# Optimization experiments

Measured on AMD Instinct MI355X. Metric: run time of the kernel, lower is better.

Reference implementation:

```python
import jax, jax.numpy as jnp
import numpy as np

B, M, N, C = 1, 128, 256, 256
MID, OUT_C = 32, 128
LN_EPS = 1e-5
NORM_EPS = 1e-3


def setup_inputs() -> dict:
    key = jax.random.key(0)
    ks = jax.random.split(key, 9)
    act = jax.random.normal(ks[0], (B, M, N, C), dtype=jnp.float32)
    mask = (jax.random.uniform(ks[1], (B, M, N)) < 0.9).astype(jnp.float32)
    s_in = 1.0 / np.sqrt(C)
    s_mid = 1.0 / np.sqrt(MID * MID)
    return {
        "act": act,
        "mask": mask,
        "ln_g": jnp.ones((C,), jnp.float32),
        "ln_b": jnp.zeros((C,), jnp.float32),
        "lw": jax.random.normal(ks[2], (MID, C), jnp.float32) * s_in,
        "lb": jnp.zeros((MID,), jnp.float32),
        "rw": jax.random.normal(ks[3], (MID, C), jnp.float32) * s_in,
        "rb": jnp.zeros((MID,), jnp.float32),
        "ow": jax.random.normal(ks[4], (OUT_C, MID * MID), jnp.float32) * s_mid,
        "ob": jnp.zeros((OUT_C,), jnp.float32),
    }


def reference(act, mask, ln_g, ln_b, lw, lb, rw, rb, ow, ob):
    # LayerNorm over channel dim
    mu = jnp.mean(act, axis=-1, keepdims=True)
    var = jnp.mean(jnp.square(act - mu), axis=-1, keepdims=True)
    x = (act - mu) * jax.lax.rsqrt(var + LN_EPS) * ln_g + ln_b  # [b,m,i,c]

    m = mask[..., None]  # [b,m,i,1]
    left = m * (jnp.einsum('bmic,xc->bmix', x, lw) + lb)   # [b,m,i,mid]
    right = m * (jnp.einsum('bmic,yc->bmiy', x, rw) + rb)  # [b,m,i,mid]

    # outer product mean over MSA dim m -> [b,i,j,x,y]
    x2d = jnp.einsum('bmix,bmjy->bijxy', left, right)
    x2d = x2d.reshape(x2d.shape[:3] + (MID * MID,))
    out = jnp.einsum('bijk,ok->bijo', x2d, ow) + ob  # [b,i,j,out_c]

    norm = jnp.einsum('bmi,bmj->bij', mask, mask)[..., None]
    return out / (norm + NORM_EPS)
```

## Files before the change

kernel.cpp:

```cpp
#include <hip/hip_runtime.h>
#include <hip/hip_bf16.h>

typedef __bf16 bf16x8 __attribute__((ext_vector_type(8)));
typedef __bf16 bf16x4 __attribute__((ext_vector_type(4)));
typedef float  f32x4  __attribute__((ext_vector_type(4)));

#define MDIM 128
#define NDIM 256
#define CDIM 256
#define MIDC 32
#define OUTC 128

#define LSX_RS 1156
#define LSX_YS 36
#define LSX_BYTES (64 * LSX_RS * 2)

__global__ __launch_bounds__(256) void prep_kernel(
    const float* __restrict__ mask,
    const float* __restrict__ lw, const float* __restrict__ lb,
    const float* __restrict__ rw, const float* __restrict__ rb,
    const float* __restrict__ ow,
    __bf16* __restrict__ wb, float* __restrict__ cbias,
    __bf16* __restrict__ owb_f, float* __restrict__ norm_inv)
{
    int b = blockIdx.x, t = threadIdx.x;
    if (b < 256) {
        float s = 0.f;
        #pragma unroll 8
        for (int m = 0; m < MDIM; ++m)
            s += mask[m*NDIM + b] * mask[m*NDIM + t];
        norm_inv[b*NDIM + t] = 1.0f / (s + 1e-3f);
    } else if (b < 320) {
        int e0 = (b - 256)*2048 + t*8;
        #pragma unroll
        for (int j = 0; j < 8; ++j) {
            int e = e0 + j;
            int idx = e >> 3, jj = e & 7;
            int lane = idx & 63, tk = idx >> 6;
            int ks = tk & 31, ot = tk >> 5;
            int o = ot*16 + (lane & 15);
            int k = ((lane >> 4)*8 + jj)*32 + ks;
            owb_f[e] = (__bf16)ow[o*1024 + k];
        }
    } else {
        int e0 = (b - 320)*2048 + t*8;
        #pragma unroll
        for (int j = 0; j < 8; ++j) {
            int e = e0 + j;
            int row = e >> 8, c = e & 255;
            wb[e] = (__bf16)(row < MIDC ? lw[row*CDIM + c] : rw[(row - MIDC)*CDIM + c]);
        }
        if (b == 320 && t < 64) cbias[t] = (t < MIDC) ? lb[t] : rb[t - MIDC];
    }
}

__global__ __launch_bounds__(256) void ln_proj_kernel(
    const float* __restrict__ act, const float* __restrict__ mask,
    const float* __restrict__ ln_g, const float* __restrict__ ln_b,
    const __bf16* __restrict__ wb, const float* __restrict__ cbias,
    __bf16* __restrict__ left_f, __bf16* __restrict__ right_f)
{
    __shared__ __bf16 xls[64][264];
    __shared__ __bf16 T[64][72];
    int t = threadIdx.x, lane = t & 63, w = t >> 6;
    int quad = lane >> 4, l16 = lane & 15;
    int b  = blockIdx.x;
    int m0 = blockIdx.y * 64;

    float4 gv = *(const float4*)(ln_g + lane*4);
    float4 bv = *(const float4*)(ln_b + lane*4);
    const float inv_c = 1.0f / 256.0f;

    #pragma unroll 4
    for (int s = 0; s < 16; ++s) {
        int m = m0 + w*16 + s;
        float4 v = *(const float4*)(act + ((size_t)m*NDIM + b)*CDIM + lane*4);
        float sum = v.x + v.y + v.z + v.w;
        float ssq = v.x*v.x + v.y*v.y + v.z*v.z + v.w*v.w;
        #pragma unroll
        for (int d = 1; d < 64; d <<= 1) {
            sum += __shfl_xor(sum, d);
            ssq += __shfl_xor(ssq, d);
        }
        float mu   = sum * inv_c;
        float var  = ssq * inv_c - mu*mu;
        float rstd = rsqrtf(var + 1e-5f);
        bf16x4 o;
        o.x = (__bf16)((v.x - mu)*rstd*gv.x + bv.x);
        o.y = (__bf16)((v.y - mu)*rstd*gv.y + bv.y);
        o.z = (__bf16)((v.z - mu)*rstd*gv.z + bv.z);
        o.w = (__bf16)((v.w - mu)*rstd*gv.w + bv.w);
        *(bf16x4*)&xls[w*16 + s][lane*4] = o;
    }

    f32x4 acc[4] = {};
    const __bf16* arow = &xls[w*16 + l16][0];
    #pragma unroll
    for (int k0 = 0; k0 < 256; k0 += 32) {
        bf16x8 a = *(const bf16x8*)(arow + k0 + quad*8);
        #pragma unroll
        for (int tt = 0; tt < 4; ++tt) {
            bf16x8 bb = *(const bf16x8*)(wb + (size_t)(tt*16 + l16)*CDIM + k0 + quad*8);
            acc[tt] = __builtin_amdgcn_mfma_f32_16x16x32_bf16(a, bb, acc[tt], 0, 0, 0);
        }
    }

    #pragma unroll
    for (int rg = 0; rg < 4; ++rg) {
        int ml = w*16 + quad*4 + rg;
        float mval = mask[(size_t)(m0 + ml)*NDIM + b];
        #pragma unroll
        for (int tt = 0; tt < 4; ++tt) {
            int o = tt*16 + l16;
            T[o][ml] = (__bf16)(mval * (acc[tt][rg] + cbias[o]));
        }
    }
    __syncthreads();

    {
        int fl16  = t & 15;
        int r     = t >> 4;
        int q     = r & 3;
        int k0loc = (r >> 2) & 1;
        int half  = (r >> 3) & 1;
        int tile  = b*2 + half;
        int k0    = (m0 >> 5) + k0loc;
        size_t dstoff = (((size_t)tile*4 + k0)*64 + q*16 + fl16)*8;
        #pragma unroll
        for (int side = 0; side < 2; ++side) {
            int o = side*32 + half*16 + fl16;
            bf16x8 d = *(const bf16x8*)&T[o][k0loc*32 + q*8];
            __bf16* dst = side ? right_f : left_f;
            *(bf16x8*)(dst + dstoff) = d;
        }
    }
}

__global__ __launch_bounds__(1024, 1) void outer_kernel(
    const __bf16* __restrict__ left_f, const __bf16* __restrict__ right_f,
    const __bf16* __restrict__ owb_f, const float* __restrict__ ob,
    const float* __restrict__ norm_inv, float* __restrict__ out)
{
    extern __shared__ __bf16 lsX[];
    int t = threadIdx.x, lane = t & 63, w = t >> 6;
    int quad = lane >> 4, l16 = lane & 15;

    int id = blockIdx.x;
    int xcd = id & 7, p = id >> 3;
    int bi = xcd*4 + (p & 3);
    int bj = p >> 2;

    int wr = w & 3, wc = w >> 2;
    const __bf16* Af = left_f  + ((size_t)(bi*16 + wr*4)*4)*512 + lane*8;
    const __bf16* Bf = right_f + ((size_t)(bj*16 + wc*4)*4)*512 + lane*8;

    f32x4 acc1[4][4] = {};
    #pragma unroll
    for (int kk = 0; kk < 4; ++kk) {
        bf16x8 af[4], bg[4];
        #pragma unroll
        for (int tr = 0; tr < 4; ++tr) af[tr] = *(const bf16x8*)(Af + tr*2048 + kk*512);
        #pragma unroll
        for (int tc = 0; tc < 4; ++tc) bg[tc] = *(const bf16x8*)(Bf + tc*2048 + kk*512);
        #pragma unroll
        for (int tr = 0; tr < 4; ++tr)
            #pragma unroll
            for (int tc = 0; tc < 4; ++tc)
                acc1[tr][tc] = __builtin_amdgcn_mfma_f32_16x16x32_bf16(af[tr], bg[tc], acc1[tr][tc], 0, 0, 0);
    }

    int ot = w & 7, rt = w >> 3;
    const __bf16* Ob = owb_f + ((size_t)(ot*32)*64 + lane)*8;
    bf16x8 bbuf0 = *(const bf16x8*)(Ob);
    bf16x8 bbuf1 = *(const bf16x8*)(Ob + 512);

    #pragma unroll
    for (int tr = 0; tr < 4; ++tr) {
        int il = wr*2 + (tr >> 1);
        int x0 = (tr & 1)*16 + quad*4;
        #pragma unroll
        for (int tc = 0; tc < 4; ++tc) {
            int jl = wc*2 + (tc >> 1);
            int y  = (tc & 1)*16 + l16;
            bf16x4 pk;
            pk.x = (__bf16)acc1[tr][tc][0];
            pk.y = (__bf16)acc1[tr][tc][1];
            pk.z = (__bf16)acc1[tr][tc][2];
            pk.w = (__bf16)acc1[tr][tc][3];
            *(bf16x4*)(lsX + (size_t)(il*8 + jl)*LSX_RS + y*LSX_YS + x0) = pk;
        }
    }
    __syncthreads();

    f32x4 acc2[2] = {};
    const __bf16* Xb = lsX + (size_t)(rt*32 + l16)*LSX_RS + quad*8;
    #pragma unroll
    for (int ks = 0; ks < 32; ++ks) {
        bf16x8 bb = bbuf0;
        bbuf0 = bbuf1;
        if (ks + 2 < 32) bbuf1 = *(const bf16x8*)(Ob + (ks + 2)*512);
        #pragma unroll
        for (int mt = 0; mt < 2; ++mt) {
            const __bf16* ap = Xb + mt*16*LSX_RS + ks*LSX_YS;
            bf16x4 lo = *(const bf16x4*)(ap);
            bf16x4 hi = *(const bf16x4*)(ap + 4);
            bf16x8 a  = __builtin_shufflevector(lo, hi, 0, 1, 2, 3, 4, 5, 6, 7);
            acc2[mt] = __builtin_amdgcn_mfma_f32_16x16x32_bf16(a, bb, acc2[mt], 0, 0, 0);
        }
    }

    int o = ot*16 + l16;
    float obv = ob[o];
    #pragma unroll
    for (int mt = 0; mt < 2; ++mt) {
        #pragma unroll
        for (int rg = 0; rg < 4; ++rg) {
            int ij = rt*32 + mt*16 + quad*4 + rg;
            int i = bi*8 + (ij >> 3), j = bj*8 + (ij & 7);
            float v = (acc2[mt][rg] + obv) * norm_inv[i*NDIM + j];
            out[((size_t)(i*NDIM + j))*OUTC + o] = v;
        }
    }
}

extern "C" void kernel_launch(void* const* d_in, const int* in_sizes, int n_in,
                              void* d_out, int out_size, void* d_ws, size_t ws_size,
                              hipStream_t stream) {
    const float* act  = (const float*)d_in[0];
    const float* mask = (const float*)d_in[1];
    const float* ln_g = (const float*)d_in[2];
    const float* ln_b = (const float*)d_in[3];
    const float* lw   = (const float*)d_in[4];
    const float* lb   = (const float*)d_in[5];
    const float* rw   = (const float*)d_in[6];
    const float* rb   = (const float*)d_in[7];
    const float* ow   = (const float*)d_in[8];
    const float* ob   = (const float*)d_in[9];
    float* out = (float*)d_out;

    unsigned char* ws = (unsigned char*)d_ws;
    __bf16* left_f   = (__bf16*)(ws + 0);
    __bf16* right_f  = (__bf16*)(ws + (2u<<20));
    __bf16* owb_f    = (__bf16*)(ws + (4u<<20));
    float*  norm_inv = (float*) (ws + (4u<<20) + (256u<<10));
    __bf16* wb       = (__bf16*)(ws + (4u<<20) + (512u<<10));
    float*  cbias    = (float*) (ws + (4u<<20) + (544u<<10));

    hipFuncSetAttribute((const void*)outer_kernel,
                        hipFuncAttributeMaxDynamicSharedMemorySize, LSX_BYTES);

    prep_kernel<<<328, 256, 0, stream>>>(mask, lw, lb, rw, rb, ow,
                                         wb, cbias, owb_f, norm_inv);
    ln_proj_kernel<<<dim3(256, 2), 256, 0, stream>>>(act, mask, ln_g, ln_b,
                                                     wb, cbias, left_f, right_f);
    outer_kernel<<<1024, 1024, LSX_BYTES, stream>>>(left_f, right_f, owb_f, ob,
                                                    norm_inv, out);
}
```

Measured before the change: 158.5 us.

## Stage left/right tiles in LDS and split-K second GEMM with 32x32 MFMA

The outer kernel first copies the block's left and right fragments into shared memory cooperatively, then feeds the first GEMM from LDS instead of per-wave global loads. The second GEMM switches from 16x16x32 to 32x32x16 MFMA, with waves split into 4 output tiles by 4 K-quarters. The K-quarter partials are reduced through an LDS scratch before one wave group writes the output. The output-weight prep layout is rewritten to match. This adds extra barriers and an LDS reduction pass, and leaves only a quarter of the waves doing the epilogue.

```diff
diff --git a/kernel.cpp b/kernel.cpp
--- a/kernel.cpp
+++ b/kernel.cpp
@@ -4,6 +4,7 @@
 typedef __bf16 bf16x8 __attribute__((ext_vector_type(8)));
 typedef __bf16 bf16x4 __attribute__((ext_vector_type(4)));
 typedef float  f32x4  __attribute__((ext_vector_type(4)));
+typedef float  f32x16 __attribute__((ext_vector_type(16)));
 
 #define MDIM 128
 #define NDIM 256
@@ -33,14 +34,15 @@
     } else if (b < 320) {
         int e0 = (b - 256)*2048 + t*8;
         #pragma unroll
-        for (int j = 0; j < 8; ++j) {
-            int e = e0 + j;
-            int idx = e >> 3, jj = e & 7;
-            int lane = idx & 63, tk = idx >> 6;
-            int ks = tk & 31, ot = tk >> 5;
-            int o = ot*16 + (lane & 15);
-            int k = ((lane >> 4)*8 + jj)*32 + ks;
-            owb_f[e] = (__bf16)ow[o*1024 + k];
+        for (int jj = 0; jj < 8; ++jj) {
+            int e = e0 + jj;
+            int lane = (e >> 3) & 63;
+            int s = (e >> 9) & 63;
+            int ot = e >> 15;
+            int o = ot*32 + (lane & 31);
+            int x = (s & 1)*16 + (lane >> 5)*8 + jj;
+            int y = s >> 1;
+            owb_f[e] = (__bf16)ow[o*1024 + x*32 + y];
         }
     } else {
         int e0 = (b - 320)*2048 + t*8;
@@ -144,24 +146,38 @@
     extern __shared__ __bf16 lsX[];
     int t = threadIdx.x, lane = t & 63, w = t >> 6;
     int quad = lane >> 4, l16 = lane & 15;
+    int l31 = lane & 31, half = lane >> 5;
 
     int id = blockIdx.x;
     int xcd = id & 7, p = id >> 3;
     int bi = xcd*4 + (p & 3);
     int bj = p >> 2;
 
+    {
+        uint4* ls4 = (uint4*)lsX;
+        const uint4* gA4 = (const uint4*)(left_f  + (size_t)bi*32768);
+        const uint4* gB4 = (const uint4*)(right_f + (size_t)bj*32768);
+        #pragma unroll
+        for (int r = 0; r < 4; ++r) ls4[r*1024 + t]        = gA4[r*1024 + t];
+        #pragma unroll
+        for (int r = 0; r < 4; ++r) ls4[4096 + r*1024 + t] = gB4[r*1024 + t];
+    }
+    __syncthreads();
+
     int wr = w & 3, wc = w >> 2;
-    const __bf16* Af = left_f  + ((size_t)(bi*16 + wr*4)*4)*512 + lane*8;
-    const __bf16* Bf = right_f + ((size_t)(bj*16 + wc*4)*4)*512 + lane*8;
+    const __bf16* lsA = lsX;
+    const __bf16* lsB = lsX + 32768;
 
     f32x4 acc1[4][4] = {};
     #pragma unroll
     for (int kk = 0; kk < 4; ++kk) {
         bf16x8 af[4], bg[4];
         #pragma unroll
-        for (int tr = 0; tr < 4; ++tr) af[tr] = *(const bf16x8*)(Af + tr*2048 + kk*512);
-        #pragma unroll
-        for (int tc = 0; tc < 4; ++tc) bg[tc] = *(const bf16x8*)(Bf + tc*2048 + kk*512);
+        for (int tr = 0; tr < 4; ++tr)
+            af[tr] = *(const bf16x8*)(lsA + (size_t)(((wr*4 + tr)*4 + kk)*512) + lane*8);
+        #pragma unroll
+        for (int tc = 0; tc < 4; ++tc)
+            bg[tc] = *(const bf16x8*)(lsB + (size_t)(((wc*4 + tc)*4 + kk)*512) + lane*8);
         #pragma unroll
         for (int tr = 0; tr < 4; ++tr)
             #pragma unroll
@@ -169,10 +185,12 @@
                 acc1[tr][tc] = __builtin_amdgcn_mfma_f32_16x16x32_bf16(af[tr], bg[tc], acc1[tr][tc], 0, 0, 0);
     }
 
-    int ot = w & 7, rt = w >> 3;
-    const __bf16* Ob = owb_f + ((size_t)(ot*32)*64 + lane)*8;
+    int ot = w & 3, kq = w >> 2;
+    const __bf16* Ob = owb_f + ((size_t)(ot*64 + kq*16)*64 + lane)*8;
     bf16x8 bbuf0 = *(const bf16x8*)(Ob);
     bf16x8 bbuf1 = *(const bf16x8*)(Ob + 512);
+
+    __syncthreads();
 
     #pragma unroll
     for (int tr = 0; tr < 4; ++tr) {
@@ -192,33 +210,55 @@
     }
     __syncthreads();
 
-    f32x4 acc2[2] = {};
-    const __bf16* Xb = lsX + (size_t)(rt*32 + l16)*LSX_RS + quad*8;
-    #pragma unroll
-    for (int ks = 0; ks < 32; ++ks) {
+    f32x16 acc2[2] = {};
+    const __bf16* Xb = lsX + (size_t)l31*LSX_RS + half*8;
+    #pragma unroll 4
+    for (int ss = 0; ss < 16; ++ss) {
+        int s = kq*16 + ss;
         bf16x8 bb = bbuf0;
         bbuf0 = bbuf1;
-        if (ks + 2 < 32) bbuf1 = *(const bf16x8*)(Ob + (ks + 2)*512);
-        #pragma unroll
-        for (int mt = 0; mt < 2; ++mt) {
-            const __bf16* ap = Xb + mt*16*LSX_RS + ks*LSX_YS;
+        if (ss + 2 < 16) bbuf1 = *(const bf16x8*)(Ob + (ss + 2)*512);
+        int xoff = (s >> 1)*LSX_YS + (s & 1)*16;
+        #pragma unroll
+        for (int rt = 0; rt < 2; ++rt) {
+            const __bf16* ap = Xb + (size_t)rt*32*LSX_RS + xoff;
             bf16x4 lo = *(const bf16x4*)(ap);
             bf16x4 hi = *(const bf16x4*)(ap + 4);
             bf16x8 a  = __builtin_shufflevector(lo, hi, 0, 1, 2, 3, 4, 5, 6, 7);
-            acc2[mt] = __builtin_amdgcn_mfma_f32_16x16x32_bf16(a, bb, acc2[mt], 0, 0, 0);
-        }
-    }
-
-    int o = ot*16 + l16;
-    float obv = ob[o];
-    #pragma unroll
-    for (int mt = 0; mt < 2; ++mt) {
-        #pragma unroll
-        for (int rg = 0; rg < 4; ++rg) {
-            int ij = rt*32 + mt*16 + quad*4 + rg;
-            int i = bi*8 + (ij >> 3), j = bj*8 + (ij & 7);
-            float v = (acc2[mt][rg] + obv) * norm_inv[i*NDIM + j];
-            out[((size_t)(i*NDIM + j))*OUTC + o] = v;
+            acc2[rt] = __builtin_amdgcn_mfma_f32_32x32x16_bf16(a, bb, acc2[rt], 0, 0, 0);
+        }
+    }
+
+    __syncthreads();
+
+    float* scr = (float*)lsX;
+    if (kq > 0) {
+        int base = (kq - 1)*8192 + ot*2048;
+        #pragma unroll
+        for (int rt = 0; rt < 2; ++rt) {
+            #pragma unroll
+            for (int r = 0; r < 16; ++r) {
+                int row = (r & 3) + 8*(r >> 2) + 4*half;
+                scr[base + rt*1024 + row*32 + l31] = acc2[rt][r];
+            }
+        }
+    }
+    __syncthreads();
+
+    if (kq == 0) {
+        int o = ot*32 + l31;
+        float obv = ob[o];
+        #pragma unroll
+        for (int rt = 0; rt < 2; ++rt) {
+            #pragma unroll
+            for (int r = 0; r < 16; ++r) {
+                int row = (r & 3) + 8*(r >> 2) + 4*half;
+                int idx = ot*2048 + rt*1024 + row*32 + l31;
+                float v = acc2[rt][r] + scr[idx] + scr[8192 + idx] + scr[16384 + idx];
+                int ij = rt*32 + row;
+                int i = bi*8 + (ij >> 3), j = bj*8 + (ij & 7);
+                out[((size_t)(i*NDIM + j))*OUTC + o] = (v + obv) * norm_inv[i*NDIM + j];
+            }
         }
     }
 }
```

Result: faster. 153.3 us (-3.3%).
